# Kernel optimization log

Hardware: AMD Instinct MI355X
Metric: run time of the kernel (lower is better)

Reference implementation:

```python
import jax, jax.numpy as jnp
import numpy as np

N_PER_CLOUD = 2048   # points per cloud (batch entries are equal-sized, sorted)
NUM_CLOUDS = 8       # batch_size constant in the source module
RADIUS = 0.2         # init arg r
MAX_NEIGHBORS = 32   # init arg max_neighbors
F_IN, H1, H2, F_OUT = 3, 64, 64, 128  # PointNet++ SA MLP widths; nn input = F_IN + 3


def setup_inputs() -> dict:
    key = jax.random.key(0)
    ks = jax.random.split(key, 8)
    N = NUM_CLOUDS * N_PER_CLOUD
    x = jax.random.normal(ks[0], (N, F_IN), dtype=jnp.float32)
    pos = jax.random.uniform(ks[1], (N, 3), dtype=jnp.float32)  # unit cube
    batch = jnp.repeat(jnp.arange(NUM_CLOUDS, dtype=jnp.int32), N_PER_CLOUD)
    d_in = F_IN + 3
    W1 = jax.random.normal(ks[2], (d_in, H1), dtype=jnp.float32) / np.sqrt(d_in)
    b1 = jnp.zeros((H1,), dtype=jnp.float32)
    W2 = jax.random.normal(ks[3], (H1, H2), dtype=jnp.float32) / np.sqrt(H1)
    b2 = jnp.zeros((H2,), dtype=jnp.float32)
    W3 = jax.random.normal(ks[4], (H2, F_OUT), dtype=jnp.float32) / np.sqrt(H2)
    b3 = jnp.zeros((F_OUT,), dtype=jnp.float32)
    return dict(x=x, pos=pos, batch=batch, W1=W1, b1=b1, W2=W2, b2=b2, W3=W3, b3=b3)


def reference(x, pos, batch, W1, b1, W2, b2, W3, b3):
    N = pos.shape[0]
    B = N // N_PER_CLOUD
    n = N_PER_CLOUD
    posb = pos.reshape(B, n, 3)
    xb = x.reshape(B, n, -1)

    # --- radius ball query (per cloud, first MAX_NEIGHBORS in index order) ---
    diff = posb[:, :, None, :] - posb[:, None, :, :]          # [B, n_query, n_src, 3]
    d2 = jnp.sum(diff * diff, axis=-1)                        # [B, n, n]
    valid = d2 <= RADIUS * RADIUS                             # includes self -> >=1 nbr
    j_idx = jnp.arange(n, dtype=jnp.int32)
    keys = jnp.where(valid, j_idx[None, None, :], n)          # invalid -> sentinel n
    nbr = jnp.argsort(keys, axis=-1)[..., :MAX_NEIGHBORS]     # [B, n, K]
    nbr_ok = jnp.take_along_axis(keys, nbr, axis=-1) < n      # [B, n, K] bool

    # --- PointNetConv: msg = nn(cat([x_j, pos_j - pos_i])), max aggregation ---
    b_ix = jnp.arange(B)[:, None, None]
    x_j = xb[b_ix, nbr]                                        # [B, n, K, F_IN]
    rel = posb[b_ix, nbr] - posb[:, :, None, :]               # [B, n, K, 3]
    msg = jnp.concatenate([x_j, rel], axis=-1)                # [B, n, K, F_IN+3]
    h = jax.nn.relu(msg @ W1 + b1)
    h = jax.nn.relu(h @ W2 + b2)
    h = h @ W3 + b3                                           # [B, n, K, F_OUT]
    h = jnp.where(nbr_ok[..., None], h, -jnp.inf)
    out = jnp.max(h, axis=2).reshape(N, -1)                   # [N, F_OUT]
    return out, pos, batch
```

## Files before the change

### kernel.cpp

```cpp
#include <hip/hip_runtime.h>
#include <hip/hip_bf16.h>
#include <math.h>

#define NPC   2048
#define NC    8
#define NTOT  (NPC * NC)
#define KMAX  32
#define R2    0.04f

typedef short bf16x8  __attribute__((ext_vector_type(8)));
typedef float f32x16  __attribute__((ext_vector_type(16)));

__device__ __forceinline__ unsigned int f2bf(float f) {
    unsigned int u = __float_as_uint(f);
    return (u + 0x7FFFu + ((u >> 16) & 1u)) >> 16;
}

__device__ __forceinline__ unsigned int pkbf(float a, float b) {
    unsigned int r;
    asm("v_cvt_pk_bf16_f32 %0, %1, %2" : "=v"(r) : "v"(a), "v"(b));
    return r;
}

__device__ __forceinline__ bf16x8 mk_frag(const f32x16& a, int off) {
    int4 w;
    w.x = (int)pkbf(fmaxf(a[off+0],0.f), fmaxf(a[off+1],0.f));
    w.y = (int)pkbf(fmaxf(a[off+2],0.f), fmaxf(a[off+3],0.f));
    w.z = (int)pkbf(fmaxf(a[off+4],0.f), fmaxf(a[off+5],0.f));
    w.w = (int)pkbf(fmaxf(a[off+6],0.f), fmaxf(a[off+7],0.f));
    return __builtin_bit_cast(bf16x8, w);
}

__global__ __launch_bounds__(512) void prep_small(
    const float* __restrict__ pos, const int* __restrict__ batch,
    const float* __restrict__ W1, const float* __restrict__ b1,
    const float* __restrict__ W2, const float* __restrict__ b2,
    const float* __restrict__ W3,
    unsigned short* __restrict__ wf, float* __restrict__ out)
{
    int b = blockIdx.x, tid = threadIdx.x;
    if (b < 28) {
        int g = b * 512 + tid;
        if (g < 1024) {
            int j = g & 7, lane = (g >> 3) & 63, t = g >> 9;
            int k = (lane >> 5)*8 + j, ch = t*32 + (lane & 31);
            float v = (k < 6) ? W1[k*64 + ch] : (k == 6 ? b1[ch] : 0.f);
            wf[g] = (unsigned short)f2bf(v);
        } else if (g < 6144) {
            int g2 = g - 1024;
            int j = g2 & 7, lane = (g2 >> 3) & 63, f = g2 >> 9;
            int t = f / 5, kk = f % 5;
            int hi = lane >> 5, row = t*32 + (lane & 31);
            float v;
            if (kk < 4) {
                int k = (j & 3) + 4*hi + 8*(2*(kk & 1) + (j >> 2)) + 32*(kk >> 1);
                v = W2[k*64 + row];
            } else {
                v = (hi == 0 && j == 0) ? b2[row] : 0.f;
            }
            wf[g] = (unsigned short)f2bf(v);
        } else {
            int g3 = g - 6144;
            int j = g3 & 7, lane = (g3 >> 3) & 63, f = g3 >> 9;
            int n = f >> 2, kk = f & 3;
            int hi = lane >> 5, col = n*32 + (lane & 31);
            int k = (j & 3) + 4*hi + 8*(2*(kk & 1) + (j >> 2)) + 32*(kk >> 1);
            wf[g] = (unsigned short)f2bf(W3[k*128 + col]);
        }
    } else {
        int i = (b - 28) * 512 + tid;
        if (i < NTOT*3) out[NTOT*128 + i] = pos[i];
        else            out[NTOT*131 + (i - NTOT*3)] = (float)batch[i - NTOT*3];
    }
}

__global__ __launch_bounds__(512, 4) void fused_kernel(
    const float* __restrict__ x, const float* __restrict__ pos,
    const unsigned short* __restrict__ wf, const float* __restrict__ b3,
    float* __restrict__ out)
{
    __shared__ float4 sP[NPC];
    __shared__ int4   sW[1664];
    __shared__ int    snbr[8*32];

    const int tid  = threadIdx.x;
    const int lane = tid & 63, wave = tid >> 6;
    const int e = lane & 31, hi = lane >> 5;
    const int blk   = blockIdx.x;
    const int base  = (blk >> 8) << 11;
    const int q     = blk * 8 + wave;
    const int ql    = q - base;

    {
        const float4* src = (const float4*)(pos + 3*base);
        float4 f0 = src[3*tid], f1 = src[3*tid+1], f2 = src[3*tid+2];
        sP[4*tid+0] = make_float4(f0.x, f0.y, f0.z, 0.f);
        sP[4*tid+1] = make_float4(f0.w, f1.x, f1.y, 0.f);
        sP[4*tid+2] = make_float4(f1.z, f1.w, f2.x, 0.f);
        sP[4*tid+3] = make_float4(f2.y, f2.z, f2.w, 0.f);
    }
    const int4* wsrc = (const int4*)(wf + 1024);
    #pragma unroll
    for (int it = 0; it < 4; ++it) {
        int idx = it*512 + tid;
        if (idx < 1664) sW[idx] = wsrc[idx];
    }
    bf16x8 wA1_0 = *(const bf16x8*)(wf + (0*64 + lane)*8);
    bf16x8 wA1_1 = *(const bf16x8*)(wf + (1*64 + lane)*8);
    float b3v[4];
    #pragma unroll
    for (int n = 0; n < 4; ++n) b3v[n] = b3[n*32 + e];
    __syncthreads();

    const float4 qp = sP[ql];
    const float qx = qp.x, qy = qp.y, qz = qp.z;
    int cnt = 0;
    for (int j0 = 0; j0 < NPC && cnt < KMAX; j0 += 256) {
        unsigned long long ms[4];
        bool vs[4];
        #pragma unroll
        for (int s = 0; s < 4; ++s) {
            float4 p = sP[j0 + s*64 + lane];
            float dx = __fsub_rn(p.x, qx);
            float dy = __fsub_rn(p.y, qy);
            float dz = __fsub_rn(p.z, qz);
            float d2 = __fadd_rn(__fadd_rn(__fmul_rn(dx,dx), __fmul_rn(dy,dy)),
                                 __fmul_rn(dz,dz));
            vs[s] = d2 <= R2;
            ms[s] = __ballot(vs[s]);
        }
        #pragma unroll
        for (int s = 0; s < 4; ++s) {
            int before = (int)__popcll(ms[s] & ((1ull << lane) - 1ull));
            int slot = cnt + before;
            if (vs[s] && slot < KMAX) snbr[(wave << 5) + slot] = j0 + s*64 + lane;
            cnt += (int)__popcll(ms[s]);
        }
    }
    if (cnt > KMAX) cnt = KMAX;
    __syncthreads();

    int jl = (e < cnt) ? snbr[(wave << 5) + e] : ql;
    float4 pj = sP[jl];
    float xj0 = x[3*(base + jl)], xj1 = x[3*(base + jl) + 1], xj2 = x[3*(base + jl) + 2];

    const unsigned int one_w = pkbf(1.0f, 0.0f);
    int4 ow = {0,0,0,0};
    if (!hi) ow.x = (int)one_w;
    const bf16x8 onef = __builtin_bit_cast(bf16x8, ow);

    float r0 = pj.x - qx, r1 = pj.y - qy, r2 = pj.z - qz;
    int4 mw;
    mw.x = hi ? 0 : (int)pkbf(xj0, xj1);
    mw.y = hi ? 0 : (int)pkbf(xj2, r0);
    mw.z = hi ? 0 : (int)pkbf(r1, r2);
    mw.w = hi ? 0 : (int)one_w;
    bf16x8 msgf = __builtin_bit_cast(bf16x8, mw);

    f32x16 acc0 = {}, acc1 = {};
    acc0 = __builtin_amdgcn_mfma_f32_32x32x16_bf16(wA1_0, msgf, acc0, 0, 0, 0);
    acc1 = __builtin_amdgcn_mfma_f32_32x32x16_bf16(wA1_1, msgf, acc1, 0, 0, 0);
    bf16x8 h1f[4];
    h1f[0] = mk_frag(acc0, 0);
    h1f[1] = mk_frag(acc0, 8);
    h1f[2] = mk_frag(acc1, 0);
    h1f[3] = mk_frag(acc1, 8);

    f32x16 c20 = {}, c21 = {};
    #pragma unroll
    for (int kk = 0; kk < 4; ++kk) {
        c20 = __builtin_amdgcn_mfma_f32_32x32x16_bf16(
                *(const bf16x8*)&sW[(0*5 + kk)*64 + lane], h1f[kk], c20, 0, 0, 0);
        c21 = __builtin_amdgcn_mfma_f32_32x32x16_bf16(
                *(const bf16x8*)&sW[(1*5 + kk)*64 + lane], h1f[kk], c21, 0, 0, 0);
    }
    c20 = __builtin_amdgcn_mfma_f32_32x32x16_bf16(
            *(const bf16x8*)&sW[(0*5 + 4)*64 + lane], onef, c20, 0, 0, 0);
    c21 = __builtin_amdgcn_mfma_f32_32x32x16_bf16(
            *(const bf16x8*)&sW[(1*5 + 4)*64 + lane], onef, c21, 0, 0, 0);
    bf16x8 h2f[4];
    h2f[0] = mk_frag(c20, 0);
    h2f[1] = mk_frag(c20, 8);
    h2f[2] = mk_frag(c21, 0);
    h2f[3] = mk_frag(c21, 8);

    const bool full = (cnt == 32);
    #pragma unroll
    for (int n = 0; n < 4; ++n) {
        f32x16 c = {};
        #pragma unroll
        for (int kk = 0; kk < 4; ++kk)
            c = __builtin_amdgcn_mfma_f32_32x32x16_bf16(
                    h2f[kk], *(const bf16x8*)&sW[640 + (n*4 + kk)*64 + lane], c, 0, 0, 0);
        float m;
        if (full) {
            m = fmaxf(fmaxf(fmaxf(c[0],c[1]), fmaxf(c[2],c[3])),
                      fmaxf(fmaxf(c[4],c[5]), fmaxf(c[6],c[7])));
            m = fmaxf(m, fmaxf(fmaxf(c[8],c[9]),  fmaxf(c[10],c[11])));
            m = fmaxf(m, fmaxf(fmaxf(c[12],c[13]), fmaxf(c[14],c[15])));
        } else {
            m = -INFINITY;
            #pragma unroll
            for (int reg = 0; reg < 16; ++reg) {
                int r = (reg & 3) + 8*(reg >> 2) + 4*hi;
                m = fmaxf(m, (r < cnt) ? c[reg] : -INFINITY);
            }
        }
        m = fmaxf(m, __shfl_xor(m, 32));
        m += b3v[n];
        if (hi == 0) out[q*128 + n*32 + e] = m;
    }
}

extern "C" void kernel_launch(void* const* d_in, const int* in_sizes, int n_in,
                              void* d_out, int out_size, void* d_ws, size_t ws_size,
                              hipStream_t stream) {
    const float* x     = (const float*)d_in[0];
    const float* pos   = (const float*)d_in[1];
    const int*   batch = (const int*)d_in[2];
    const float* W1    = (const float*)d_in[3];
    const float* b1    = (const float*)d_in[4];
    const float* W2    = (const float*)d_in[5];
    const float* b2    = (const float*)d_in[6];
    const float* W3    = (const float*)d_in[7];
    const float* b3    = (const float*)d_in[8];
    float* out = (float*)d_out;

    unsigned short* wfrag = (unsigned short*)d_ws;

    prep_small<<<156, 512, 0, stream>>>(pos, batch, W1, b1, W2, b2, W3, wfrag, out);
    fused_kernel<<<2048, 512, 0, stream>>>(x, pos, wfrag, b3, out);
}
```

Before: 43.34 us.

## Split shared positions into xy/z arrays, drop block barrier, add MFMA priority hints

Stores the per-cloud point positions in shared memory as a float2 xy array plus a separate float z array, cutting LDS use from 32 KB to 24 KB per block. Raises the launch-bounds occupancy hint from 4 to 6 blocks. Removes the __syncthreads after the ball query, since each wave only reads its own neighbour slots, and brackets the MFMA chains with s_setprio to favour matrix issue across waves. The trade-off is two LDS loads per point instead of one in the distance scan, and a tighter register budget that could cause spills.

```diff
diff --git a/kernel.cpp b/kernel.cpp
--- a/kernel.cpp
+++ b/kernel.cpp
@@ -74,12 +74,13 @@
     }
 }
 
-__global__ __launch_bounds__(512, 4) void fused_kernel(
+__global__ __launch_bounds__(512, 6) void fused_kernel(
     const float* __restrict__ x, const float* __restrict__ pos,
     const unsigned short* __restrict__ wf, const float* __restrict__ b3,
     float* __restrict__ out)
 {
-    __shared__ float4 sP[NPC];
+    __shared__ float2 sPxy[NPC];
+    __shared__ float  sPz[NPC];
     __shared__ int4   sW[1664];
     __shared__ int    snbr[8*32];
 
@@ -94,10 +95,10 @@
     {
         const float4* src = (const float4*)(pos + 3*base);
         float4 f0 = src[3*tid], f1 = src[3*tid+1], f2 = src[3*tid+2];
-        sP[4*tid+0] = make_float4(f0.x, f0.y, f0.z, 0.f);
-        sP[4*tid+1] = make_float4(f0.w, f1.x, f1.y, 0.f);
-        sP[4*tid+2] = make_float4(f1.z, f1.w, f2.x, 0.f);
-        sP[4*tid+3] = make_float4(f2.y, f2.z, f2.w, 0.f);
+        sPxy[4*tid+0] = make_float2(f0.x, f0.y); sPz[4*tid+0] = f0.z;
+        sPxy[4*tid+1] = make_float2(f0.w, f1.x); sPz[4*tid+1] = f1.y;
+        sPxy[4*tid+2] = make_float2(f1.z, f1.w); sPz[4*tid+2] = f2.x;
+        sPxy[4*tid+3] = make_float2(f2.y, f2.z); sPz[4*tid+3] = f2.w;
     }
     const int4* wsrc = (const int4*)(wf + 1024);
     #pragma unroll
@@ -112,18 +113,20 @@
     for (int n = 0; n < 4; ++n) b3v[n] = b3[n*32 + e];
     __syncthreads();
 
-    const float4 qp = sP[ql];
-    const float qx = qp.x, qy = qp.y, qz = qp.z;
+    const float2 qxy = sPxy[ql];
+    const float qx = qxy.x, qy = qxy.y, qz = sPz[ql];
     int cnt = 0;
     for (int j0 = 0; j0 < NPC && cnt < KMAX; j0 += 256) {
         unsigned long long ms[4];
         bool vs[4];
         #pragma unroll
         for (int s = 0; s < 4; ++s) {
-            float4 p = sP[j0 + s*64 + lane];
-            float dx = __fsub_rn(p.x, qx);
-            float dy = __fsub_rn(p.y, qy);
-            float dz = __fsub_rn(p.z, qz);
+            int j = j0 + s*64 + lane;
+            float2 pxy = sPxy[j];
+            float  pz  = sPz[j];
+            float dx = __fsub_rn(pxy.x, qx);
+            float dy = __fsub_rn(pxy.y, qy);
+            float dz = __fsub_rn(pz,    qz);
             float d2 = __fadd_rn(__fadd_rn(__fmul_rn(dx,dx), __fmul_rn(dy,dy)),
                                  __fmul_rn(dz,dz));
             vs[s] = d2 <= R2;
@@ -138,10 +141,10 @@
         }
     }
     if (cnt > KMAX) cnt = KMAX;
-    __syncthreads();
 
     int jl = (e < cnt) ? snbr[(wave << 5) + e] : ql;
-    float4 pj = sP[jl];
+    float2 pjxy = sPxy[jl];
+    float  pjz  = sPz[jl];
     float xj0 = x[3*(base + jl)], xj1 = x[3*(base + jl) + 1], xj2 = x[3*(base + jl) + 2];
 
     const unsigned int one_w = pkbf(1.0f, 0.0f);
@@ -149,7 +152,7 @@
     if (!hi) ow.x = (int)one_w;
     const bf16x8 onef = __builtin_bit_cast(bf16x8, ow);
 
-    float r0 = pj.x - qx, r1 = pj.y - qy, r2 = pj.z - qz;
+    float r0 = pjxy.x - qx, r1 = pjxy.y - qy, r2 = pjz - qz;
     int4 mw;
     mw.x = hi ? 0 : (int)pkbf(xj0, xj1);
     mw.y = hi ? 0 : (int)pkbf(xj2, r0);
@@ -157,15 +160,18 @@
     mw.w = hi ? 0 : (int)one_w;
     bf16x8 msgf = __builtin_bit_cast(bf16x8, mw);
 
+    __builtin_amdgcn_s_setprio(1);
     f32x16 acc0 = {}, acc1 = {};
     acc0 = __builtin_amdgcn_mfma_f32_32x32x16_bf16(wA1_0, msgf, acc0, 0, 0, 0);
     acc1 = __builtin_amdgcn_mfma_f32_32x32x16_bf16(wA1_1, msgf, acc1, 0, 0, 0);
+    __builtin_amdgcn_s_setprio(0);
     bf16x8 h1f[4];
     h1f[0] = mk_frag(acc0, 0);
     h1f[1] = mk_frag(acc0, 8);
     h1f[2] = mk_frag(acc1, 0);
     h1f[3] = mk_frag(acc1, 8);
 
+    __builtin_amdgcn_s_setprio(1);
     f32x16 c20 = {}, c21 = {};
     #pragma unroll
     for (int kk = 0; kk < 4; ++kk) {
@@ -178,6 +184,7 @@
             *(const bf16x8*)&sW[(0*5 + 4)*64 + lane], onef, c20, 0, 0, 0);
     c21 = __builtin_amdgcn_mfma_f32_32x32x16_bf16(
             *(const bf16x8*)&sW[(1*5 + 4)*64 + lane], onef, c21, 0, 0, 0);
+    __builtin_amdgcn_s_setprio(0);
     bf16x8 h2f[4];
     h2f[0] = mk_frag(c20, 0);
     h2f[1] = mk_frag(c20, 8);
@@ -187,11 +194,13 @@
     const bool full = (cnt == 32);
     #pragma unroll
     for (int n = 0; n < 4; ++n) {
+        __builtin_amdgcn_s_setprio(1);
         f32x16 c = {};
         #pragma unroll
         for (int kk = 0; kk < 4; ++kk)
             c = __builtin_amdgcn_mfma_f32_32x32x16_bf16(
                     h2f[kk], *(const bf16x8*)&sW[640 + (n*4 + kk)*64 + lane], c, 0, 0, 0);
+        __builtin_amdgcn_s_setprio(0);
         float m;
         if (full) {
             m = fmaxf(fmaxf(fmaxf(c[0],c[1]), fmaxf(c[2],c[3])),
```

New measurement: 38.42 us. -11.4%, faster.
